# Kernel optimization log

Hardware: AMD Instinct MI355X
Metric: run time of the kernel (lower is better)

Reference implementation:

```python
import jax, jax.numpy as jnp
import numpy as np

ALPHA = 0.9          # alpha_mem
THRESHOLD = 1.0
WINDOW = 1.0         # module-level `window`; spike fn receives threshold*window
MEM_SUBTRACT = THRESHOLD  # membrane_subtract defaults to threshold


@jax.custom_vjp
def spike(v):
    # sinabs ThresholdSubtract forward: multiple spikes per step via floor division
    return jnp.where(v > 0, jnp.floor(v / THRESHOLD), 0.0)

def _spike_fwd(v):
    return spike(v), v

def _spike_bwd(v, g):
    # surrogate gradient: boxcar heaviside(v - (threshold - window)) / threshold
    grad = (v >= (THRESHOLD - THRESHOLD * WINDOW)).astype(g.dtype) / THRESHOLD
    return (g * grad,)

spike.defvjp(_spike_fwd, _spike_bwd)


def setup_inputs() -> dict:
    key = jax.random.key(0)
    k1, k2 = jax.random.split(key, 2)
    B, T, N = 32, 1000, 1024
    input_current = jax.random.normal(k1, (B, T, N), dtype=jnp.float32)
    w_rec = jax.random.normal(k2, (N, N), dtype=jnp.float32) * 0.02  # Linear weight [out, in]
    b_rec = jnp.zeros((N,), dtype=jnp.float32)
    return {"input_current": input_current, "w_rec": w_rec, "b_rec": b_rec}


def reference(input_current, w_rec, b_rec):
    B, T, N = input_current.shape

    def step(carry, x_t):
        state, rec = carry                      # [B, N] each
        total = x_t + rec                       # recurrent feedback added to input
        act = spike(state)                      # spikes from state BEFORE integration (1-step delay)
        state = state - act * MEM_SUBTRACT      # membrane subtract after spiking
        state = state * ALPHA + (1.0 - ALPHA) * total  # leaky integration
        rec = act @ w_rec.T + b_rec             # recurrent GEMM for next step
        return (state, rec), act

    state0 = jnp.zeros((B, N), dtype=input_current.dtype)
    rec0 = jnp.zeros((B, N), dtype=input_current.dtype)
    xs = jnp.swapaxes(input_current, 0, 1)      # [T, B, N]
    _, spikes = jax.lax.scan(step, (state0, rec0), xs)
    return jnp.swapaxes(spikes, 0, 1)           # [B, T, N]
```

## Files before the change

kernel.cpp:

```cpp
#include <hip/hip_runtime.h>
#include <cstdint>
#include <cstddef>

#define B_       32
#define T_       1000
#define N_       1024
#define THREADS_ 512
#define CWAVES_  4
#define CHUNK_   8
#define NCHUNK_  125
#define DEPTH_   4
#define SLOT_BYTES_ 32768
#define ZBLOCKS_ 224

typedef float v4f __attribute__((ext_vector_type(4)));

__device__ __forceinline__ v4f vmax4(v4f a, v4f b) {
  v4f r;
  r.x = fmaxf(a.x, b.x); r.y = fmaxf(a.y, b.y);
  r.z = fmaxf(a.z, b.z); r.w = fmaxf(a.w, b.w);
  return r;
}

#define DSRD(dst, base, imm)                                                 \
  asm volatile("ds_read_b128 %0, %1 offset:" #imm : "=v"(dst) : "v"(base))

#define GLD(dst, p)                                                          \
  asm volatile("global_load_dwordx4 %0, %1, off" : "=v"(dst) : "v"(p))

#define VM8 asm volatile("s_waitcnt vmcnt(8)" ::: "memory")
#define VM0 asm volatile("s_waitcnt vmcnt(0)" ::: "memory")

#define GIS(b0,b1,b2,b3,b4,b5,b6,b7, cc)                                     \
  do {                                                                       \
    const float* _p = sbase + (size_t)(cc) * (CHUNK_ * N_);                  \
    GLD(b0, _p + 0 * N_); GLD(b1, _p + 1 * N_);                              \
    GLD(b2, _p + 2 * N_); GLD(b3, _p + 3 * N_);                              \
    GLD(b4, _p + 4 * N_); GLD(b5, _p + 5 * N_);                              \
    GLD(b6, _p + 6 * N_); GLD(b7, _p + 7 * N_);                              \
    __builtin_amdgcn_sched_barrier(0);                  \
  } while (0)

#define WRS(b0,b1,b2,b3,b4,b5,b6,b7, cc)                                     \
  do {                                                                       \
    const int _sl = (cc) & (DEPTH_ - 1);                                     \
    xring[_sl][0][col] = b0; xring[_sl][1][col] = b1;                        \
    xring[_sl][2][col] = b2; xring[_sl][3][col] = b3;                        \
    xring[_sl][4][col] = b4; xring[_sl][5][col] = b5;                        \
    xring[_sl][6][col] = b6; xring[_sl][7][col] = b7;                        \
  } while (0)

#define SPEC_STEP(xf)                                                        \
  do {                                                                       \
    cmax = vmax4(cmax, st);                                                  \
    v4f _t = (xf) + rr;                                                      \
    st = st * 0.9f + 0.1f * _t;                                              \
    rr = brec;                                                               \
  } while (0)

#define PROCESS(cc)                                                          \
  do {                                                                       \
    unsigned _a = xb + (unsigned)(((cc) & (DEPTH_ - 1)) * SLOT_BYTES_)       \
                     + ((unsigned)tid << 4);                                 \
    v4f _x0, _x1, _x2, _x3, _x4, _x5, _x6, _x7;                              \
    DSRD(_x0, _a, 0);     DSRD(_x1, _a, 4096);                               \
    DSRD(_x2, _a, 8192);  DSRD(_x3, _a, 12288);                              \
    DSRD(_x4, _a, 16384); DSRD(_x5, _a, 20480);                              \
    DSRD(_x6, _a, 24576); DSRD(_x7, _a, 28672);                              \
    asm volatile("s_waitcnt lgkmcnt(0)");                                    \
    __builtin_amdgcn_sched_barrier(0);    \
    v4f st = state, rr = rec, cmax = state;                                  \
    SPEC_STEP(_x0); SPEC_STEP(_x1); SPEC_STEP(_x2); SPEC_STEP(_x3);          \
    SPEC_STEP(_x4); SPEC_STEP(_x5); SPEC_STEP(_x6); SPEC_STEP(_x7);          \
    float _m = fmaxf(fmaxf(cmax.x, cmax.y), fmaxf(cmax.z, cmax.w));          \
    int _any = (_m >= 1.0f);                                                 \
    const int _p = (cc) & 1;                                                 \
    unsigned long long _wm = __ballot(_any);                                 \
    if (lane == 0) s_cmask[_p][wv] = _wm;                                    \
    __syncthreads();                                                         \
    unsigned long long _ab =                                                 \
        s_cmask[_p][0] | s_cmask[_p][1] | s_cmask[_p][2] | s_cmask[_p][3];   \
    if (_ab == 0ULL) { state = st; rec = brec; }                             \
    else { replay(cc); }                                                     \
  } while (0)

__global__ __launch_bounds__(THREADS_, 1)
void lif_fused(const float* __restrict__ x, const float* __restrict__ w,
               const float* __restrict__ brec_g, float* __restrict__ out,
               unsigned long long* __restrict__ ws_rec,
               unsigned int* __restrict__ ws_cnt, int cap)
{
  if (blockIdx.x >= B_) {
    const size_t n4 = (size_t)B_ * T_ * N_ / 4;
    size_t i = (size_t)(blockIdx.x - B_) * THREADS_ + threadIdx.x;
    const size_t stride = (size_t)(gridDim.x - B_) * THREADS_;
    v4f* o4 = (v4f*)out;
    v4f z = (v4f)(0.f);
    for (; i < n4; i += stride) __builtin_nontemporal_store(z, &o4[i]);
    return;
  }

  const int b    = blockIdx.x;
  const int tid  = threadIdx.x;
  const int lane = tid & 63;
  const int wv   = tid >> 6;

  __shared__ v4f xring[DEPTH_][CHUNK_][N_ / 4];
  __shared__ unsigned long long s_cmask[2][CWAVES_];
  __shared__ unsigned long long s_mask [2][CWAVES_];
  __shared__ v4f                s_val  [2][CWAVES_ * 64];
  __shared__ unsigned int       s_spkcnt;

  if (tid == 0) s_spkcnt = 0;

  const float* xg_base = x + (size_t)b * T_ * N_;

  if (wv >= CWAVES_) {
    const int pw  = wv - CWAVES_;
    const int col = (pw << 6) + lane;
    const float* sbase = xg_base + ((size_t)col << 2);

    auto replaycheck = [&](int c) {
      const int p = c & 1;
      unsigned long long ab =
          s_cmask[p][0] | s_cmask[p][1] | s_cmask[p][2] | s_cmask[p][3];
      if (ab != 0ULL) {
#pragma unroll 1
        for (int k = 0; k < CHUNK_; ++k) __syncthreads();
      }
    };

    v4f A0, A1, A2, A3, A4, A5, A6, A7;
    v4f B0, B1, B2, B3, B4, B5, B6, B7;

    GIS(A0,A1,A2,A3,A4,A5,A6,A7, 0);
    GIS(B0,B1,B2,B3,B4,B5,B6,B7, 1);
    VM8; WRS(A0,A1,A2,A3,A4,A5,A6,A7, 0);
    GIS(A0,A1,A2,A3,A4,A5,A6,A7, 2);
    VM8; WRS(B0,B1,B2,B3,B4,B5,B6,B7, 1);
    GIS(B0,B1,B2,B3,B4,B5,B6,B7, 3);
    __syncthreads();

#pragma unroll 1
    for (int c = 0; c < NCHUNK_ - 1; c += 2) {
      if (c <= NCHUNK_ - 5) {
        VM8; WRS(A0,A1,A2,A3,A4,A5,A6,A7, c + 2);
        GIS(A0,A1,A2,A3,A4,A5,A6,A7, c + 4);
      } else {
        VM0; WRS(A0,A1,A2,A3,A4,A5,A6,A7, c + 2);
      }
      __syncthreads();
      replaycheck(c);
      if (c <= NCHUNK_ - 5) {
        VM8; WRS(B0,B1,B2,B3,B4,B5,B6,B7, c + 3);
        if (c <= NCHUNK_ - 7)
          GIS(B0,B1,B2,B3,B4,B5,B6,B7, c + 5);
      }
      __syncthreads();
      replaycheck(c + 1);
    }
    __syncthreads();
    replaycheck(NCHUNK_ - 1);
    __syncthreads();
    return;
  }

  __builtin_amdgcn_s_setprio(1);
  const int n0 = tid << 2;

  const unsigned xb =
      (unsigned)(uintptr_t)(__attribute__((address_space(3))) void*)xring;

  v4f state = (v4f)(0.f);
  v4f rec   = (v4f)(0.f);
  const v4f brec = *(const v4f*)(brec_g + n0);

  auto replay = [&](int cc) {
    v4f st = state;
    v4f r  = rec;
    const int sl = cc & (DEPTH_ - 1);
#pragma unroll 1
    for (int k = 0; k < CHUNK_; ++k) {
      const int q = k & 1;
      v4f xv = xring[sl][k][tid];
      float tx = xv.x + r.x, ty = xv.y + r.y, tz = xv.z + r.z, tw = xv.w + r.w;
      float ax = (st.x > 0.f) ? floorf(st.x) : 0.f;
      float ay = (st.y > 0.f) ? floorf(st.y) : 0.f;
      float az = (st.z > 0.f) ? floorf(st.z) : 0.f;
      float aw = (st.w > 0.f) ? floorf(st.w) : 0.f;
      int ms = (ax != 0.f) | (ay != 0.f) | (az != 0.f) | (aw != 0.f);
      if (ms) {
        v4f v; v.x = ax; v.y = ay; v.z = az; v.w = aw;
        s_val[q][tid] = v;
        unsigned int off = (unsigned int)((cc * CHUNK_ + k) * N_ + n0);
        float av[4] = {ax, ay, az, aw};
#pragma unroll
        for (int e = 0; e < 4; ++e) {
          if (av[e] != 0.f) {
            unsigned int idx = atomicAdd(&s_spkcnt, 1u);
            if ((int)idx < cap)
              ws_rec[(size_t)b * cap + idx] =
                  ((unsigned long long)(off + e) << 32) |
                  (unsigned long long)__float_as_uint(av[e]);
          }
        }
      }
      unsigned long long sm = __ballot(ms);
      if (lane == 0) s_mask[q][wv] = sm;
      st.x = (st.x - ax) * 0.9f + 0.1f * tx;
      st.y = (st.y - ay) * 0.9f + 0.1f * ty;
      st.z = (st.z - az) * 0.9f + 0.1f * tz;
      st.w = (st.w - aw) * 0.9f + 0.1f * tw;
      __syncthreads();
      v4f racc = brec;
#pragma unroll 1
      for (int w2 = 0; w2 < CWAVES_; ++w2) {
        unsigned long long mm = s_mask[q][w2];
        while (mm) {
          int l = __builtin_ctzll(mm);
          mm &= mm - 1;
          int j = (w2 << 6) + l;
          v4f v = s_val[q][j];
          int jn = j << 2;
          if (v.x != 0.f) {
            racc.x += v.x * w[(size_t)(n0 + 0) * N_ + jn];
            racc.y += v.x * w[(size_t)(n0 + 1) * N_ + jn];
            racc.z += v.x * w[(size_t)(n0 + 2) * N_ + jn];
            racc.w += v.x * w[(size_t)(n0 + 3) * N_ + jn];
          }
          if (v.y != 0.f) {
            int j1 = jn + 1;
            racc.x += v.y * w[(size_t)(n0 + 0) * N_ + j1];
            racc.y += v.y * w[(size_t)(n0 + 1) * N_ + j1];
            racc.z += v.y * w[(size_t)(n0 + 2) * N_ + j1];
            racc.w += v.y * w[(size_t)(n0 + 3) * N_ + j1];
          }
          if (v.z != 0.f) {
            int j2 = jn + 2;
            racc.x += v.z * w[(size_t)(n0 + 0) * N_ + j2];
            racc.y += v.z * w[(size_t)(n0 + 1) * N_ + j2];
            racc.z += v.z * w[(size_t)(n0 + 2) * N_ + j2];
            racc.w += v.z * w[(size_t)(n0 + 3) * N_ + j2];
          }
          if (v.w != 0.f) {
            int j3 = jn + 3;
            racc.x += v.w * w[(size_t)(n0 + 0) * N_ + j3];
            racc.y += v.w * w[(size_t)(n0 + 1) * N_ + j3];
            racc.z += v.w * w[(size_t)(n0 + 2) * N_ + j3];
            racc.w += v.w * w[(size_t)(n0 + 3) * N_ + j3];
          }
        }
      }
      r = racc;
    }
    state = st;
    rec   = r;
  };

  __syncthreads();
#pragma unroll 1
  for (int c = 0; c < NCHUNK_; ++c) {
    PROCESS(c);
  }

  __syncthreads();
  if (tid == 0) ws_cnt[b] = s_spkcnt;
}

__global__ void scatter_spikes(const unsigned long long* __restrict__ rec,
                               const unsigned int* __restrict__ cnt,
                               float* __restrict__ out, int cap)
{
  int b = blockIdx.x;
  unsigned int n = cnt[b];
  if ((int)n > cap) n = cap;
  for (unsigned int i = threadIdx.x; i < n; i += blockDim.x) {
    unsigned long long r = rec[(size_t)b * cap + i];
    unsigned int off = (unsigned int)(r >> 32);
    float v = __uint_as_float((unsigned int)r);
    out[(size_t)b * (T_ * N_) + off] = v;
  }
}

extern "C" void kernel_launch(void* const* d_in, const int* in_sizes, int n_in,
                              void* d_out, int out_size, void* d_ws, size_t ws_size,
                              hipStream_t stream) {
  const float* x  = (const float*)d_in[0];
  const float* w  = (const float*)d_in[1];
  const float* br = (const float*)d_in[2];
  float* out = (float*)d_out;

  int cap = 4096;
  size_t need = (size_t)B_ * cap * 8 + B_ * 4;
  if (ws_size < need && ws_size > 256)
    cap = (int)((ws_size - 256) / ((size_t)B_ * 8));
  unsigned long long* rec = (unsigned long long*)d_ws;
  unsigned int* cnt = (unsigned int*)((char*)d_ws + (size_t)B_ * cap * 8);

  lif_fused<<<B_ + ZBLOCKS_, THREADS_, 0, stream>>>(x, w, br, out, rec, cnt, cap);
  scatter_spikes<<<B_, THREADS_, 0, stream>>>(rec, cnt, out, cap);
}
```

Baseline: 326.3 us.

## Assign whole chunks to producer waves with contiguous row loads

Changes the producer-wave loading scheme so that each of the four producer waves owns every fourth chunk, loading all 8 rows of that chunk with contiguous 1 KB row segments (four dwordx4 loads per row at offsets). Previously each wave loaded a column slice of every chunk. The new scheme issues 32 loads per wave per owned chunk, holding them in 32 vector registers, and waits with vmcnt(0) before writing them to the LDS ring. The intent is to make global reads more contiguous per wave and to let each wave keep more loads in flight across several chunk periods. In exchange it raises register pressure and uses a coarser wait.

```diff
diff --git a/kernel.cpp b/kernel.cpp
--- a/kernel.cpp
+++ b/kernel.cpp
@@ -25,29 +25,52 @@
 #define DSRD(dst, base, imm)                                                 \
   asm volatile("ds_read_b128 %0, %1 offset:" #imm : "=v"(dst) : "v"(base))
 
-#define GLD(dst, p)                                                          \
-  asm volatile("global_load_dwordx4 %0, %1, off" : "=v"(dst) : "v"(p))
-
-#define VM8 asm volatile("s_waitcnt vmcnt(8)" ::: "memory")
-#define VM0 asm volatile("s_waitcnt vmcnt(0)" ::: "memory")
-
-#define GIS(b0,b1,b2,b3,b4,b5,b6,b7, cc)                                     \
-  do {                                                                       \
-    const float* _p = sbase + (size_t)(cc) * (CHUNK_ * N_);                  \
-    GLD(b0, _p + 0 * N_); GLD(b1, _p + 1 * N_);                              \
-    GLD(b2, _p + 2 * N_); GLD(b3, _p + 3 * N_);                              \
-    GLD(b4, _p + 4 * N_); GLD(b5, _p + 5 * N_);                              \
-    GLD(b6, _p + 6 * N_); GLD(b7, _p + 7 * N_);                              \
+#define GROW(d0,d1,d2,d3, p)                                                 \
+  asm volatile("global_load_dwordx4 %0, %4, off\n\t"                         \
+               "global_load_dwordx4 %1, %4, off offset:1024\n\t"             \
+               "global_load_dwordx4 %2, %4, off offset:2048\n\t"             \
+               "global_load_dwordx4 %3, %4, off offset:3072"                 \
+               : "=&v"(d0), "=&v"(d1), "=&v"(d2), "=&v"(d3) : "v"(p))
+
+#define GIS32(cc)                                                            \
+  do {                                                                       \
+    const float* _pr = sbase + (size_t)(cc) * (CHUNK_ * N_);                 \
+    GROW(P00,P01,P02,P03, _pr + 0 * N_);                                     \
+    GROW(P10,P11,P12,P13, _pr + 1 * N_);                                     \
+    GROW(P20,P21,P22,P23, _pr + 2 * N_);                                     \
+    GROW(P30,P31,P32,P33, _pr + 3 * N_);                                     \
+    GROW(P40,P41,P42,P43, _pr + 4 * N_);                                     \
+    GROW(P50,P51,P52,P53, _pr + 5 * N_);                                     \
+    GROW(P60,P61,P62,P63, _pr + 6 * N_);                                     \
+    GROW(P70,P71,P72,P73, _pr + 7 * N_);                                     \
     __builtin_amdgcn_sched_barrier(0);                  \
   } while (0)
 
-#define WRS(b0,b1,b2,b3,b4,b5,b6,b7, cc)                                     \
+#define WRS32(cc)                                                            \
   do {                                                                       \
     const int _sl = (cc) & (DEPTH_ - 1);                                     \
-    xring[_sl][0][col] = b0; xring[_sl][1][col] = b1;                        \
-    xring[_sl][2][col] = b2; xring[_sl][3][col] = b3;                        \
-    xring[_sl][4][col] = b4; xring[_sl][5][col] = b5;                        \
-    xring[_sl][6][col] = b6; xring[_sl][7][col] = b7;                        \
+    xring[_sl][0][lane] = P00; xring[_sl][0][lane+64] = P01;                 \
+    xring[_sl][0][lane+128] = P02; xring[_sl][0][lane+192] = P03;            \
+    xring[_sl][1][lane] = P10; xring[_sl][1][lane+64] = P11;                 \
+    xring[_sl][1][lane+128] = P12; xring[_sl][1][lane+192] = P13;            \
+    xring[_sl][2][lane] = P20; xring[_sl][2][lane+64] = P21;                 \
+    xring[_sl][2][lane+128] = P22; xring[_sl][2][lane+192] = P23;            \
+    xring[_sl][3][lane] = P30; xring[_sl][3][lane+64] = P31;                 \
+    xring[_sl][3][lane+128] = P32; xring[_sl][3][lane+192] = P33;            \
+    xring[_sl][4][lane] = P40; xring[_sl][4][lane+64] = P41;                 \
+    xring[_sl][4][lane+128] = P42; xring[_sl][4][lane+192] = P43;            \
+    xring[_sl][5][lane] = P50; xring[_sl][5][lane+64] = P51;                 \
+    xring[_sl][5][lane+128] = P52; xring[_sl][5][lane+192] = P53;            \
+    xring[_sl][6][lane] = P60; xring[_sl][6][lane+64] = P61;                 \
+    xring[_sl][6][lane+128] = P62; xring[_sl][6][lane+192] = P63;            \
+    xring[_sl][7][lane] = P70; xring[_sl][7][lane+64] = P71;                 \
+    xring[_sl][7][lane+128] = P72; xring[_sl][7][lane+192] = P73;            \
+  } while (0)
+
+#define VM0W                                                                 \
+  do {                                                                       \
+    asm volatile("s_waitcnt vmcnt(0)" ::: "memory");                         \
+    __builtin_amdgcn_sched_barrier(0);    \
   } while (0)
 
 #define SPEC_STEP(xf)                                                        \
@@ -116,9 +139,8 @@
   const float* xg_base = x + (size_t)b * T_ * N_;
 
   if (wv >= CWAVES_) {
-    const int pw  = wv - CWAVES_;
-    const int col = (pw << 6) + lane;
-    const float* sbase = xg_base + ((size_t)col << 2);
+    const int pw = wv - CWAVES_;
+    const float* sbase = xg_base + ((size_t)lane << 2);
 
     auto replaycheck = [&](int c) {
       const int p = c & 1;
@@ -130,37 +152,28 @@
       }
     };
 
-    v4f A0, A1, A2, A3, A4, A5, A6, A7;
-    v4f B0, B1, B2, B3, B4, B5, B6, B7;
-
-    GIS(A0,A1,A2,A3,A4,A5,A6,A7, 0);
-    GIS(B0,B1,B2,B3,B4,B5,B6,B7, 1);
-    VM8; WRS(A0,A1,A2,A3,A4,A5,A6,A7, 0);
-    GIS(A0,A1,A2,A3,A4,A5,A6,A7, 2);
-    VM8; WRS(B0,B1,B2,B3,B4,B5,B6,B7, 1);
-    GIS(B0,B1,B2,B3,B4,B5,B6,B7, 3);
+    v4f P00,P01,P02,P03, P10,P11,P12,P13, P20,P21,P22,P23, P30,P31,P32,P33,
+        P40,P41,P42,P43, P50,P51,P52,P53, P60,P61,P62,P63, P70,P71,P72,P73;
+
+    GIS32(pw);
+    if (pw < 2) {
+      VM0W;
+      WRS32(pw);
+      GIS32(pw + 4);
+    }
     __syncthreads();
 
 #pragma unroll 1
-    for (int c = 0; c < NCHUNK_ - 1; c += 2) {
-      if (c <= NCHUNK_ - 5) {
-        VM8; WRS(A0,A1,A2,A3,A4,A5,A6,A7, c + 2);
-        GIS(A0,A1,A2,A3,A4,A5,A6,A7, c + 4);
-      } else {
-        VM0; WRS(A0,A1,A2,A3,A4,A5,A6,A7, c + 2);
+    for (int c = 0; c < NCHUNK_; ++c) {
+      const int wr = c + 2;
+      if ((wr & 3) == pw && wr < NCHUNK_) {
+        VM0W;
+        WRS32(wr);
+        if (wr + 4 < NCHUNK_) GIS32(wr + 4);
       }
       __syncthreads();
       replaycheck(c);
-      if (c <= NCHUNK_ - 5) {
-        VM8; WRS(B0,B1,B2,B3,B4,B5,B6,B7, c + 3);
-        if (c <= NCHUNK_ - 7)
-          GIS(B0,B1,B2,B3,B4,B5,B6,B7, c + 5);
-      }
-      __syncthreads();
-      replaycheck(c + 1);
     }
-    __syncthreads();
-    replaycheck(NCHUNK_ - 1);
     __syncthreads();
     return;
   }
```

Result: no change. 330.1 us (+1.1%).
